# Kernel tuning notes

Hardware: AMD Instinct MI355X
Metric: run time of the kernel (lower is better)

## Reference

```python
import jax, jax.numpy as jnp
import numpy as np

NEG_SLOPE = 0.2
NUM_NODES = 100000
NUM_EDGES = 200000
NNZ = 1600000
IN_C = 128
OUT_C = 128
STAR = 64


def setup_inputs() -> dict:
    key = jax.random.key(0)
    ks = jax.random.split(key, 12)
    X = jax.random.normal(ks[0], (NUM_NODES, IN_C), dtype=jnp.float32)
    V = jax.random.randint(ks[1], (NNZ,), 0, NUM_NODES)
    E = jax.random.randint(ks[2], (NNZ,), 0, NUM_EDGES)
    S_features = jax.random.normal(ks[3], (NUM_EDGES, STAR), dtype=jnp.float32)
    s = 1.0 / np.sqrt(IN_C)
    Wx = jax.random.uniform(ks[4], (IN_C, OUT_C), minval=-s, maxval=s)
    bx = jax.random.uniform(ks[5], (OUT_C,), minval=-s, maxval=s)
    Wv = jax.random.uniform(ks[6], (IN_C, OUT_C), minval=-s, maxval=s)
    bv = jax.random.uniform(ks[7], (OUT_C,), minval=-s, maxval=s)
    sa = 1.0 / np.sqrt(OUT_C)
    a_vec = jax.random.uniform(ks[8], (OUT_C,), minval=-sa, maxval=sa)
    st = 1.0 / np.sqrt(OUT_C + STAR)
    Wt = jax.random.uniform(ks[9], (OUT_C + STAR, OUT_C), minval=-st, maxval=st)
    bt = jax.random.uniform(ks[10], (OUT_C,), minval=-st, maxval=st)
    return {"X": X, "V": V, "E": E, "S_features": S_features,
            "Wx": Wx, "bx": bx, "Wv": Wv, "bv": bv,
            "a_vec": a_vec, "Wt": Wt, "bt": bt}


def _segment_softmax(s, seg, num_segments):
    m = jax.ops.segment_max(s, seg, num_segments=num_segments)
    e = jnp.exp(s - m[seg])
    denom = jax.ops.segment_sum(e, seg, num_segments=num_segments)
    return e / denom[seg]


def reference(X, V, E, S_features, Wx, bx, Wv, bv, a_vec, Wt, bt):
    # DPHGNNConv forward (eval mode: dropout = identity)
    X_init = X @ Wx + bx                      # [N, out]
    X_feat = X @ Wv + bv                      # [N, out]
    scores = X_feat @ a_vec                   # [N]
    s = jax.nn.leaky_relu(scores[V], NEG_SLOPE)  # [nnz]
    w = _segment_softmax(s, E, NUM_EDGES)     # [nnz]
    Xev = X_feat[V] * w[:, None]              # [nnz, out]
    Y_v2e = jax.ops.segment_sum(Xev, E, num_segments=NUM_EDGES)
    Y_v2e = jax.nn.elu(Y_v2e)
    e_msg = jnp.concatenate([Y_v2e, S_features], axis=1)  # [E, out+star]
    Y = e_msg @ Wt + bt                       # [E, out]
    Yev = Y[E]                                # [nnz, out]
    num = jax.ops.segment_sum(Yev, V, num_segments=NUM_NODES)
    cnt = jax.ops.segment_sum(jnp.ones((NNZ,), jnp.float32), V, num_segments=NUM_NODES)
    Xn = num / jnp.maximum(cnt, 1.0)[:, None]  # scatter_mean
    Xn = jax.nn.elu(Xn)                        # is_last=False
    return Xn + X_init
```

## Files before the change

kernel.cpp:

```cpp
#include <hip/hip_runtime.h>
#include <math.h>

#define N_NODES 100000
#define N_EDGES 200000
#define NNZ_    1600000
#define INC  128
#define OUTC 128
#define STAR_ 64
#define NEG 0.2f
#define NBIN_E 391
#define NBIN_V 196
#define NBIN (NBIN_E + NBIN_V)
#define CHUNK 4000
#define CAP_E 5120
#define CAP_V 9216
#define PAIR_SZ (NBIN_E*CAP_E + NBIN_V*CAP_V)
#define CAPI 288

typedef __attribute__((ext_vector_type(8))) short bf16x8_t;
typedef __attribute__((ext_vector_type(4))) float f32x4_t;

__device__ __forceinline__ float leaky(float x){ return x > 0.f ? x : NEG*x; }
__device__ __forceinline__ float elu1(float x){ return x > 0.f ? x : __expf(x)-1.f; }
__device__ __forceinline__ unsigned short f2bf(float f){
  unsigned u = __float_as_uint(f);
  unsigned r = u + 0x7FFFu + ((u >> 16) & 1u);
  return (unsigned short)(r >> 16);
}
__device__ __forceinline__ float bf2f(unsigned short h){
  return __uint_as_float(((unsigned)h) << 16);
}
__device__ __forceinline__ int padBaseD(int bin){
  return bin < NBIN_E ? bin*CAP_E : NBIN_E*CAP_E + (bin-NBIN_E)*CAP_V;
}

__global__ void k_cvt(const float* __restrict__ Wx, const float* __restrict__ Wv,
                      const float* __restrict__ Wt,
                      unsigned short* __restrict__ WcatT, unsigned short* __restrict__ WtT,
                      int* __restrict__ binCur){
  const int i = blockIdx.x*256 + threadIdx.x;
  if (i < 256*128){
    const int n = i >> 7, k = i & 127;
    const float v = (n < 128) ? Wx[k*128 + n] : Wv[k*128 + (n-128)];
    WcatT[n*128 + k] = f2bf(v);
  }
  const int j = i - 256*128;
  if (j >= 0 && j < 128*192){
    const int n = j / 192, k = j - n*192;
    WtT[n*192 + k] = f2bf(Wt[k*128 + n]);
  }
  if (blockIdx.x == 0){
    for (int p = threadIdx.x; p < NBIN; p += 256) binCur[p] = padBaseD(p);
  }
}

__global__ __launch_bounds__(256) void k_gemm1(const float* __restrict__ X,
    const unsigned short* __restrict__ WcatT,
    const float* __restrict__ bx, const float* __restrict__ bv,
    float* __restrict__ Xinit, unsigned short* __restrict__ Xfb){
  __shared__ unsigned short xb[16][136];
  const int tid = threadIdx.x;
  const int lane = tid & 63, w = tid >> 6;
  const int quad = lane >> 4, l16 = lane & 15;
  const int r0 = blockIdx.x * 16;
  {
    const int r = tid >> 4;
    const int c0 = (tid & 15) * 8;
    const float4 a4 = *(const float4*)&X[(size_t)(r0+r)*INC + c0];
    const float4 b4 = *(const float4*)&X[(size_t)(r0+r)*INC + c0 + 4];
    bf16x8_t pk;
    pk[0]=(short)f2bf(a4.x); pk[1]=(short)f2bf(a4.y); pk[2]=(short)f2bf(a4.z); pk[3]=(short)f2bf(a4.w);
    pk[4]=(short)f2bf(b4.x); pk[5]=(short)f2bf(b4.y); pk[6]=(short)f2bf(b4.z); pk[7]=(short)f2bf(b4.w);
    *(bf16x8_t*)&xb[r][c0] = pk;
  }
  __syncthreads();
  f32x4_t acc[4] = {{0,0,0,0},{0,0,0,0},{0,0,0,0},{0,0,0,0}};
  const int n_base = w*64 + l16;
  for (int s = 0; s < 4; ++s){
    const bf16x8_t af = *(const bf16x8_t*)&xb[l16][s*32 + quad*8];
    #pragma unroll
    for (int nt = 0; nt < 4; ++nt){
      const int n = n_base + nt*16;
      const bf16x8_t bf = *(const bf16x8_t*)&WcatT[(size_t)n*128 + s*32 + quad*8];
      acc[nt] = __builtin_amdgcn_mfma_f32_16x16x32_bf16(af, bf, acc[nt], 0, 0, 0);
    }
  }
  #pragma unroll
  for (int nt = 0; nt < 4; ++nt){
    const int n = n_base + nt*16;
    const float bias = (n < 128) ? bx[n] : bv[n-128];
    #pragma unroll
    for (int r = 0; r < 4; ++r){
      const int m = quad*4 + r;
      const float val = acc[nt][r] + bias;
      if (n < 128) Xinit[(size_t)(r0+m)*OUTC + n] = val;
      else         Xfb[(size_t)(r0+m)*OUTC + (n-128)] = f2bf(val);
    }
  }
}

__global__ __launch_bounds__(256) void k_scores(const unsigned short* __restrict__ Xfb,
    const float* __restrict__ a, float* __restrict__ scores){
  const int lane = threadIdx.x & 63;
  const int w = threadIdx.x >> 6;
  const int r = blockIdx.x * 4 + w;
  const unsigned pair = *(const unsigned*)&Xfb[(size_t)r*OUTC + lane*2];
  float p = bf2f((unsigned short)(pair & 0xffff)) * a[lane*2]
          + bf2f((unsigned short)(pair >> 16))    * a[lane*2+1];
  #pragma unroll
  for (int o = 32; o; o >>= 1) p += __shfl_xor(p, o, 64);
  if (lane == 0) scores[r] = p;
}


__global__ __launch_bounds__(256) void k_binA(const int* __restrict__ V, const int* __restrict__ E,
                                              int* __restrict__ binCur, int2* __restrict__ pair){
  __shared__ int h[NBIN];
  __shared__ int base[NBIN];
  for (int p = threadIdx.x; p < NBIN; p += 256) h[p] = 0;
  __syncthreads();
  const int start = blockIdx.x*CHUNK, end = start + CHUNK;
  for (int i = start + threadIdx.x; i < end; i += 256){
    atomicAdd(&h[E[i] >> 9], 1);
    atomicAdd(&h[NBIN_E + (V[i] >> 9)], 1);
  }
  __syncthreads();
  for (int p = threadIdx.x; p < NBIN; p += 256)
    base[p] = h[p] ? atomicAdd(&binCur[p], h[p]) : 0;
  __syncthreads();
  for (int p = threadIdx.x; p < NBIN; p += 256) h[p] = 0;
  __syncthreads();
  for (int i = start + threadIdx.x; i < end; i += 256){
    const int e = E[i], v = V[i];
    const int be = e >> 9, bv = NBIN_E + (v >> 9);
    const int se = base[be] + atomicAdd(&h[be], 1);
    const int sv = base[bv] + atomicAdd(&h[bv], 1);
    pair[se] = make_int2(e, v);
    pair[sv] = make_int2(v, e);
  }
}

__global__ __launch_bounds__(1024) void k_binscan(const int* __restrict__ binCur,
                                                  int* __restrict__ binBase, int* __restrict__ binCnt,
                                                  int2* __restrict__ vw, int* __restrict__ eIdxV){
  __shared__ int s[1024];
  const int tid = threadIdx.x;
  const int v = (tid < NBIN) ? (binCur[tid] - padBaseD(tid)) : 0;
  s[tid] = v; __syncthreads();
  for (int o = 1; o < 1024; o <<= 1){
    const int u = (tid >= o) ? s[tid-o] : 0;
    __syncthreads();
    s[tid] += u;
    __syncthreads();
  }
  if (tid < NBIN){ binBase[tid] = s[tid] - v; binCnt[tid] = v; }
  if (tid < 16){ vw[NNZ_ + tid] = make_int2(0, 0); eIdxV[NNZ_ + tid] = 0; }
}

__global__ __launch_bounds__(256) void k_binB(const int2* __restrict__ pair,
    const int* __restrict__ binBase, const int* __restrict__ binCnt,
    const float* __restrict__ scores,
    int2* __restrict__ vw, int* __restrict__ eIdxV,
    int* __restrict__ cntE, int* __restrict__ startsE,
    int* __restrict__ cntV, int* __restrict__ startsV,
    float* __restrict__ dens){
  __shared__ int h[512], sc0[512], sc1[512];
  __shared__ float dsh[512];
  const int bin = blockIdx.x;
  const bool isE = bin < NBIN_E;
  const int nb = isE ? bin : bin - NBIN_E;
  const int bucket0 = nb << 9;
  const int nBuckTot = isE ? N_EDGES : N_NODES;
  const int pstart = padBaseD(bin);
  const int n = binCnt[bin];
  const int itemBase = isE ? binBase[bin] : binBase[bin] - NNZ_;
  const int tid = threadIdx.x;
  for (int p = tid; p < 512; p += 256){ h[p] = 0; dsh[p] = 0.f; }
  __syncthreads();
  for (int j = tid; j < n; j += 256) atomicAdd(&h[pair[pstart + j].x & 511], 1);
  __syncthreads();
  for (int p = tid; p < 512; p += 256) sc0[p] = h[p];
  __syncthreads();
  int* a = sc0; int* b = sc1;
  for (int o = 1; o < 512; o <<= 1){
    for (int p = tid; p < 512; p += 256) b[p] = a[p] + (p >= o ? a[p-o] : 0);
    __syncthreads();
    int* t = a; a = b; b = t;
  }
  for (int p = tid; p < 512; p += 256){
    const int excl = a[p] - h[p];
    b[p] = itemBase + excl;
    const int bucket = bucket0 + p;
    if (bucket < nBuckTot){
      if (isE){ cntE[bucket] = h[p]; startsE[bucket] = itemBase + excl; }
      else    { cntV[bucket] = h[p]; startsV[bucket] = itemBase + excl; }
    }
  }
  __syncthreads();
  for (int j = tid; j < n; j += 256){
    const int2 kv = pair[pstart + j];
    const int slot = atomicAdd(&b[kv.x & 511], 1);
    if (isE){
      const float ex = __expf(leaky(scores[kv.y]));
      vw[slot] = make_int2(kv.y, __float_as_int(ex));
      atomicAdd(&dsh[kv.x & 511], ex);
    } else {
      eIdxV[slot] = kv.y;
    }
  }
  __syncthreads();
  if (isE){
    for (int p = tid; p < 512; p += 256){
      const int bucket = bucket0 + p;
      if (bucket < N_EDGES) dens[bucket] = dsh[p];
    }
  }
}

__global__ __launch_bounds__(256) void k_edge(
    const int* __restrict__ cntE, const int* __restrict__ startsE,
    const int2* __restrict__ vw, const float* __restrict__ dens,
    const unsigned short* __restrict__ Xfb,
    const float* __restrict__ S, const unsigned short* __restrict__ WtT,
    const float* __restrict__ bt, unsigned short* __restrict__ Ybf) {
  __shared__ int2 inc[CAPI + 8];
  __shared__ unsigned short msg[16][200];
  const int tid = threadIdx.x;
  const int lane = tid & 63, w = tid >> 6;
  const int e0 = blockIdx.x * 16;
  const int sub = tid & 31, grp = tid >> 5;

  const int st0 = startsE[e0];
  const int lim = startsE[e0 + 15] + cntE[e0 + 15] - st0;

  for (int i = tid; i < CAPI + 8; i += 256)
    inc[i] = (i < lim) ? vw[st0 + i] : make_int2(0, 0);

  if (sub < 16) {
    const int cs = sub * 4;
    #pragma unroll
    for (int tt = 0; tt < 2; ++tt) {
      const int t = grp*2 + tt;
      const float4 s4 = *(const float4*)&S[(size_t)(e0+t)*STAR_ + cs];
      ushort4 pk; pk.x=f2bf(s4.x); pk.y=f2bf(s4.y); pk.z=f2bf(s4.z); pk.w=f2bf(s4.w);
      *(ushort4*)&msg[t][128 + cs] = pk;
    }
  }
  __syncthreads();

  const int c4 = sub * 4;
  #pragma unroll
  for (int tt = 0; tt < 2; ++tt) {
    const int t = grp*2 + tt;
    const int e = e0 + t;
    const int deg = cntE[e];
    const int lo  = startsE[e] - st0;
    float a0=0.f, a1=0.f, a2=0.f, a3=0.f;
    if (lo + deg <= CAPI) {
      for (int j = 0; j < deg; j += 8) {
        int2 pp[8];
        #pragma unroll
        for (int k = 0; k < 8; ++k) pp[k] = inc[lo + j + k];
        ushort4 xx[8];
        #pragma unroll
        for (int k = 0; k < 8; ++k)
          xx[k] = *(const ushort4*)&Xfb[(size_t)pp[k].x*OUTC + c4];
        #pragma unroll
        for (int k = 0; k < 8; ++k) {
          const float wgt = (j + k < deg) ? __int_as_float(pp[k].y) : 0.f;
          a0 += wgt * bf2f(xx[k].x); a1 += wgt * bf2f(xx[k].y);
          a2 += wgt * bf2f(xx[k].z); a3 += wgt * bf2f(xx[k].w);
        }
      }
    } else {
      const int st = st0 + lo;
      for (int j = 0; j < deg; j += 8) {
        int2 pp[8];
        #pragma unroll
        for (int k = 0; k < 8; ++k) pp[k] = vw[st + j + k];
        ushort4 xx[8];
        #pragma unroll
        for (int k = 0; k < 8; ++k)
          xx[k] = *(const ushort4*)&Xfb[(size_t)pp[k].x*OUTC + c4];
        #pragma unroll
        for (int k = 0; k < 8; ++k) {
          const float wgt = (j + k < deg) ? __int_as_float(pp[k].y) : 0.f;
          a0 += wgt * bf2f(xx[k].x); a1 += wgt * bf2f(xx[k].y);
          a2 += wgt * bf2f(xx[k].z); a3 += wgt * bf2f(xx[k].w);
        }
      }
    }
    const float invd = deg > 0 ? 1.f/dens[e] : 0.f;
    ushort4 pk;
    pk.x = f2bf(elu1(a0*invd)); pk.y = f2bf(elu1(a1*invd));
    pk.z = f2bf(elu1(a2*invd)); pk.w = f2bf(elu1(a3*invd));
    *(ushort4*)&msg[t][c4] = pk;
  }
  __syncthreads();

  const int quad = lane >> 4, l16 = lane & 15;
  f32x4_t acc0 = {0,0,0,0}, acc1 = {0,0,0,0};
  const int n0 = w * 32;
  for (int s = 0; s < 6; ++s) {
    const bf16x8_t af = *(const bf16x8_t*)&msg[l16][s*32 + quad*8];
    const bf16x8_t b0 = *(const bf16x8_t*)&WtT[(size_t)(n0 + l16)*192      + s*32 + quad*8];
    const bf16x8_t b1 = *(const bf16x8_t*)&WtT[(size_t)(n0 + 16 + l16)*192 + s*32 + quad*8];
    acc0 = __builtin_amdgcn_mfma_f32_16x16x32_bf16(af, b0, acc0, 0, 0, 0);
    acc1 = __builtin_amdgcn_mfma_f32_16x16x32_bf16(af, b1, acc1, 0, 0, 0);
  }
  const float bt0 = bt[n0 + l16], bt1 = bt[n0 + 16 + l16];
  #pragma unroll
  for (int r = 0; r < 4; ++r) {
    const int m = quad*4 + r;
    Ybf[(size_t)(e0+m)*OUTC + n0 + l16]      = f2bf(acc0[r] + bt0);
    Ybf[(size_t)(e0+m)*OUTC + n0 + 16 + l16] = f2bf(acc1[r] + bt1);
  }
}

__global__ __launch_bounds__(256) void k_node(
    const int* __restrict__ cntV, const int* __restrict__ startsV,
    const int* __restrict__ eIdxV,
    const unsigned short* __restrict__ Ybf, float* __restrict__ out) {
  __shared__ int elds[CAPI + 8];
  const int tid = threadIdx.x;
  const int sub = tid & 31, grp = tid >> 5;
  const int v0 = blockIdx.x * 8;

  const int st0 = startsV[v0];
  const int lim = startsV[v0 + 7] + cntV[v0 + 7] - st0;
  for (int i = tid; i < CAPI + 8; i += 256)
    elds[i] = (i < lim) ? eIdxV[st0 + i] : 0;
  __syncthreads();

  const int v = v0 + grp;
  const int c4 = sub * 4;
  const int deg = cntV[v];
  const int lo  = startsV[v] - st0;
  float a0=0.f, a1=0.f, a2=0.f, a3=0.f;
  if (lo + deg <= CAPI) {
    for (int j = 0; j < deg; j += 8) {
      int ee[8];
      #pragma unroll
      for (int k = 0; k < 8; ++k) ee[k] = elds[lo + j + k];
      ushort4 yy[8];
      #pragma unroll
      for (int k = 0; k < 8; ++k)
        yy[k] = *(const ushort4*)&Ybf[(size_t)ee[k]*OUTC + c4];
      #pragma unroll
      for (int k = 0; k < 8; ++k) {
        const float pz = (j + k < deg) ? 1.f : 0.f;
        a0 += pz * bf2f(yy[k].x); a1 += pz * bf2f(yy[k].y);
        a2 += pz * bf2f(yy[k].z); a3 += pz * bf2f(yy[k].w);
      }
    }
  } else {
    const int st = st0 + lo;
    for (int j = 0; j < deg; j += 8) {
      int ee[8];
      #pragma unroll
      for (int k = 0; k < 8; ++k) ee[k] = eIdxV[st + j + k];
      ushort4 yy[8];
      #pragma unroll
      for (int k = 0; k < 8; ++k)
        yy[k] = *(const ushort4*)&Ybf[(size_t)ee[k]*OUTC + c4];
      #pragma unroll
      for (int k = 0; k < 8; ++k) {
        const float pz = (j + k < deg) ? 1.f : 0.f;
        a0 += pz * bf2f(yy[k].x); a1 += pz * bf2f(yy[k].y);
        a2 += pz * bf2f(yy[k].z); a3 += pz * bf2f(yy[k].w);
      }
    }
  }
  const float invd = 1.f / fmaxf((float)deg, 1.f);
  float4 o = *(float4*)&out[(size_t)v*OUTC + c4];
  o.x = elu1(a0*invd) + o.x;
  o.y = elu1(a1*invd) + o.y;
  o.z = elu1(a2*invd) + o.z;
  o.w = elu1(a3*invd) + o.w;
  *(float4*)&out[(size_t)v*OUTC + c4] = o;
}

extern "C" void kernel_launch(void* const* d_in, const int* in_sizes, int n_in,
                              void* d_out, int out_size, void* d_ws, size_t ws_size,
                              hipStream_t stream) {
  const float* X  = (const float*)d_in[0];
  const int*   V  = (const int*)d_in[1];
  const int*   E  = (const int*)d_in[2];
  const float* S  = (const float*)d_in[3];
  const float* Wx = (const float*)d_in[4];
  const float* bx = (const float*)d_in[5];
  const float* Wv = (const float*)d_in[6];
  const float* bv = (const float*)d_in[7];
  const float* av = (const float*)d_in[8];
  const float* Wt = (const float*)d_in[9];
  const float* bt = (const float*)d_in[10];
  float* out = (float*)d_out;

  char* ws = (char*)d_ws;
  size_t off = 0;
  auto alloc = [&](size_t bytes) -> void* {
    off = (off + 255) & ~(size_t)255;
    void* p = ws + off; off += bytes; return p;
  };
  unsigned short* Xfb   = (unsigned short*)alloc((size_t)N_NODES*OUTC*2);
  unsigned short* Ybf   = (unsigned short*)alloc((size_t)N_EDGES*OUTC*2);
  float* scores = (float*)alloc((size_t)N_NODES*4);
  unsigned short* WcatT = (unsigned short*)alloc((size_t)256*128*2);
  unsigned short* WtT   = (unsigned short*)alloc((size_t)128*192*2);
  int2* pair   = (int2*)alloc((size_t)PAIR_SZ*8);
  int* binBase = (int*)alloc((size_t)NBIN*4);
  int* binCur  = (int*)alloc((size_t)NBIN*4);
  int* binCnt  = (int*)alloc((size_t)NBIN*4);
  int* cntE    = (int*)alloc((size_t)N_EDGES*4);
  int* cntV    = (int*)alloc((size_t)N_NODES*4);
  int* startsE = (int*)alloc((size_t)N_EDGES*4);
  int* startsV = (int*)alloc((size_t)N_NODES*4);
  int2* vw     = (int2*)alloc((size_t)(NNZ_+16)*8);
  int* eIdxV   = (int*)alloc((size_t)(NNZ_+16)*4);
  float* dens  = (float*)alloc((size_t)N_EDGES*4);

  k_cvt<<<(256*128 + 128*192 + 255)/256, 256, 0, stream>>>(Wx, Wv, Wt, WcatT, WtT, binCur);
  k_gemm1<<<N_NODES/16, 256, 0, stream>>>(X, WcatT, bx, bv, out, Xfb);
  k_scores<<<N_NODES/4, 256, 0, stream>>>(Xfb, av, scores);

  k_binA<<<NNZ_/CHUNK, 256, 0, stream>>>(V, E, binCur, pair);
  k_binscan<<<1, 1024, 0, stream>>>(binCur, binBase, binCnt, vw, eIdxV);
  k_binB<<<NBIN, 256, 0, stream>>>(pair, binBase, binCnt, scores, vw, eIdxV,
                                   cntE, startsE, cntV, startsV, dens);

  k_edge<<<N_EDGES/16, 256, 0, stream>>>(cntE, startsE, vw, dens, Xfb, S, WtT, bt, Ybf);
  k_node<<<N_NODES/8, 256, 0, stream>>>(cntV, startsV, eIdxV, Ybf, out);
}
```

Measured before the change: 497.9 us.

## Fuse score dot-product into GEMM epilogue and widen gathers to 16B per lane

Removes the separate k_scores launch by computing the attention score dot product inside the k_gemm1 epilogue, using shared-memory atomics across waves. The edge and node gather kernels now use 16 lanes per row with 8-element (16-byte) bf16 loads instead of 32 lanes with 4-element loads. The node kernel also processes 16 nodes per block with a larger LDS index cache. Scores are now computed from fp32 values before bf16 rounding, which slightly changes numerics. The wider per-lane accumulators raise register pressure, and there are fewer lanes in flight per row.

```diff
diff --git a/kernel.cpp b/kernel.cpp
--- a/kernel.cpp
+++ b/kernel.cpp
@@ -16,8 +16,10 @@
 #define CAP_V 9216
 #define PAIR_SZ (NBIN_E*CAP_E + NBIN_V*CAP_V)
 #define CAPI 288
+#define CAPN 448
 
 typedef __attribute__((ext_vector_type(8))) short bf16x8_t;
+typedef __attribute__((ext_vector_type(8))) unsigned short u16x8;
 typedef __attribute__((ext_vector_type(4))) float f32x4_t;
 
 __device__ __forceinline__ float leaky(float x){ return x > 0.f ? x : NEG*x; }
@@ -57,12 +59,16 @@
 __global__ __launch_bounds__(256) void k_gemm1(const float* __restrict__ X,
     const unsigned short* __restrict__ WcatT,
     const float* __restrict__ bx, const float* __restrict__ bv,
-    float* __restrict__ Xinit, unsigned short* __restrict__ Xfb){
+    const float* __restrict__ av,
+    float* __restrict__ Xinit, unsigned short* __restrict__ Xfb,
+    float* __restrict__ scores){
   __shared__ unsigned short xb[16][136];
+  __shared__ float sc[16];
   const int tid = threadIdx.x;
   const int lane = tid & 63, w = tid >> 6;
   const int quad = lane >> 4, l16 = lane & 15;
   const int r0 = blockIdx.x * 16;
+  if (tid < 16) sc[tid] = 0.f;
   {
     const int r = tid >> 4;
     const int c0 = (tid & 15) * 8;
@@ -85,6 +91,7 @@
       acc[nt] = __builtin_amdgcn_mfma_f32_16x16x32_bf16(af, bf, acc[nt], 0, 0, 0);
     }
   }
+  float pr[4] = {0.f, 0.f, 0.f, 0.f};
   #pragma unroll
   for (int nt = 0; nt < 4; ++nt){
     const int n = n_base + nt*16;
@@ -94,22 +101,18 @@
       const int m = quad*4 + r;
       const float val = acc[nt][r] + bias;
       if (n < 128) Xinit[(size_t)(r0+m)*OUTC + n] = val;
-      else         Xfb[(size_t)(r0+m)*OUTC + (n-128)] = f2bf(val);
-    }
-  }
-}
-
-__global__ __launch_bounds__(256) void k_scores(const unsigned short* __restrict__ Xfb,
-    const float* __restrict__ a, float* __restrict__ scores){
-  const int lane = threadIdx.x & 63;
-  const int w = threadIdx.x >> 6;
-  const int r = blockIdx.x * 4 + w;
-  const unsigned pair = *(const unsigned*)&Xfb[(size_t)r*OUTC + lane*2];
-  float p = bf2f((unsigned short)(pair & 0xffff)) * a[lane*2]
-          + bf2f((unsigned short)(pair >> 16))    * a[lane*2+1];
-  #pragma unroll
-  for (int o = 32; o; o >>= 1) p += __shfl_xor(p, o, 64);
-  if (lane == 0) scores[r] = p;
+      else {
+        Xfb[(size_t)(r0+m)*OUTC + (n-128)] = f2bf(val);
+        pr[r] += val * av[n-128];
+      }
+    }
+  }
+  if (w >= 2){
+    #pragma unroll
+    for (int r = 0; r < 4; ++r) atomicAdd(&sc[quad*4 + r], pr[r]);
+  }
+  __syncthreads();
+  if (tid < 16) scores[r0 + tid] = sc[tid];
 }
 
 
@@ -228,7 +231,7 @@
   const int tid = threadIdx.x;
   const int lane = tid & 63, w = tid >> 6;
   const int e0 = blockIdx.x * 16;
-  const int sub = tid & 31, grp = tid >> 5;
+  const int g16 = tid >> 4, s16 = tid & 15;
 
   const int st0 = startsE[e0];
   const int lim = startsE[e0 + 15] + cntE[e0 + 15] - st0;
@@ -236,65 +239,58 @@
   for (int i = tid; i < CAPI + 8; i += 256)
     inc[i] = (i < lim) ? vw[st0 + i] : make_int2(0, 0);
 
-  if (sub < 16) {
-    const int cs = sub * 4;
+  {
+    const float4 s4 = *(const float4*)&S[(size_t)(e0+g16)*STAR_ + s16*4];
+    ushort4 pk; pk.x=f2bf(s4.x); pk.y=f2bf(s4.y); pk.z=f2bf(s4.z); pk.w=f2bf(s4.w);
+    *(ushort4*)&msg[g16][128 + s16*4] = pk;
+  }
+  __syncthreads();
+
+  const int e = e0 + g16;
+  const int deg = cntE[e];
+  const int lo  = startsE[e] - st0;
+  const int c8 = s16 * 8;
+  float ac[8] = {0.f,0.f,0.f,0.f,0.f,0.f,0.f,0.f};
+  if (lo + deg <= CAPI) {
+    for (int j = 0; j < deg; j += 8) {
+      int2 pp[8];
+      #pragma unroll
+      for (int k = 0; k < 8; ++k) pp[k] = inc[lo + j + k];
+      u16x8 xx[8];
+      #pragma unroll
+      for (int k = 0; k < 8; ++k)
+        xx[k] = *(const u16x8*)&Xfb[(size_t)pp[k].x*OUTC + c8];
+      #pragma unroll
+      for (int k = 0; k < 8; ++k) {
+        const float wgt = (j + k < deg) ? __int_as_float(pp[k].y) : 0.f;
+        #pragma unroll
+        for (int q = 0; q < 8; ++q) ac[q] += wgt * bf2f(xx[k][q]);
+      }
+    }
+  } else {
+    const int st = st0 + lo;
+    for (int j = 0; j < deg; j += 8) {
+      int2 pp[8];
+      #pragma unroll
+      for (int k = 0; k < 8; ++k) pp[k] = vw[st + j + k];
+      u16x8 xx[8];
+      #pragma unroll
+      for (int k = 0; k < 8; ++k)
+        xx[k] = *(const u16x8*)&Xfb[(size_t)pp[k].x*OUTC + c8];
+      #pragma unroll
+      for (int k = 0; k < 8; ++k) {
+        const float wgt = (j + k < deg) ? __int_as_float(pp[k].y) : 0.f;
+        #pragma unroll
+        for (int q = 0; q < 8; ++q) ac[q] += wgt * bf2f(xx[k][q]);
+      }
+    }
+  }
+  {
+    const float invd = deg > 0 ? 1.f/dens[e] : 0.f;
+    u16x8 pk;
     #pragma unroll
-    for (int tt = 0; tt < 2; ++tt) {
-      const int t = grp*2 + tt;
-      const float4 s4 = *(const float4*)&S[(size_t)(e0+t)*STAR_ + cs];
-      ushort4 pk; pk.x=f2bf(s4.x); pk.y=f2bf(s4.y); pk.z=f2bf(s4.z); pk.w=f2bf(s4.w);
-      *(ushort4*)&msg[t][128 + cs] = pk;
-    }
-  }
-  __syncthreads();
-
-  const int c4 = sub * 4;
-  #pragma unroll
-  for (int tt = 0; tt < 2; ++tt) {
-    const int t = grp*2 + tt;
-    const int e = e0 + t;
-    const int deg = cntE[e];
-    const int lo  = startsE[e] - st0;
-    float a0=0.f, a1=0.f, a2=0.f, a3=0.f;
-    if (lo + deg <= CAPI) {
-      for (int j = 0; j < deg; j += 8) {
-        int2 pp[8];
-        #pragma unroll
-        for (int k = 0; k < 8; ++k) pp[k] = inc[lo + j + k];
-        ushort4 xx[8];
-        #pragma unroll
-        for (int k = 0; k < 8; ++k)
-          xx[k] = *(const ushort4*)&Xfb[(size_t)pp[k].x*OUTC + c4];
-        #pragma unroll
-        for (int k = 0; k < 8; ++k) {
-          const float wgt = (j + k < deg) ? __int_as_float(pp[k].y) : 0.f;
-          a0 += wgt * bf2f(xx[k].x); a1 += wgt * bf2f(xx[k].y);
-          a2 += wgt * bf2f(xx[k].z); a3 += wgt * bf2f(xx[k].w);
-        }
-      }
-    } else {
-      const int st = st0 + lo;
-      for (int j = 0; j < deg; j += 8) {
-        int2 pp[8];
-        #pragma unroll
-        for (int k = 0; k < 8; ++k) pp[k] = vw[st + j + k];
-        ushort4 xx[8];
-        #pragma unroll
-        for (int k = 0; k < 8; ++k)
-          xx[k] = *(const ushort4*)&Xfb[(size_t)pp[k].x*OUTC + c4];
-        #pragma unroll
-        for (int k = 0; k < 8; ++k) {
-          const float wgt = (j + k < deg) ? __int_as_float(pp[k].y) : 0.f;
-          a0 += wgt * bf2f(xx[k].x); a1 += wgt * bf2f(xx[k].y);
-          a2 += wgt * bf2f(xx[k].z); a3 += wgt * bf2f(xx[k].w);
-        }
-      }
-    }
-    const float invd = deg > 0 ? 1.f/dens[e] : 0.f;
-    ushort4 pk;
-    pk.x = f2bf(elu1(a0*invd)); pk.y = f2bf(elu1(a1*invd));
-    pk.z = f2bf(elu1(a2*invd)); pk.w = f2bf(elu1(a3*invd));
-    *(ushort4*)&msg[t][c4] = pk;
+    for (int q = 0; q < 8; ++q) pk[q] = f2bf(elu1(ac[q]*invd));
+    *(u16x8*)&msg[g16][c8] = pk;
   }
   __syncthreads();
 
@@ -321,36 +317,36 @@
     const int* __restrict__ cntV, const int* __restrict__ startsV,
     const int* __restrict__ eIdxV,
     const unsigned short* __restrict__ Ybf, float* __restrict__ out) {
-  __shared__ int elds[CAPI + 8];
+  __shared__ int elds[CAPN + 8];
   const int tid = threadIdx.x;
-  const int sub = tid & 31, grp = tid >> 5;
-  const int v0 = blockIdx.x * 8;
+  const int g16 = tid >> 4, s16 = tid & 15;
+  const int v0 = blockIdx.x * 16;
 
   const int st0 = startsV[v0];
-  const int lim = startsV[v0 + 7] + cntV[v0 + 7] - st0;
-  for (int i = tid; i < CAPI + 8; i += 256)
+  const int lim = startsV[v0 + 15] + cntV[v0 + 15] - st0;
+  for (int i = tid; i < CAPN + 8; i += 256)
     elds[i] = (i < lim) ? eIdxV[st0 + i] : 0;
   __syncthreads();
 
-  const int v = v0 + grp;
-  const int c4 = sub * 4;
+  const int v = v0 + g16;
   const int deg = cntV[v];
   const int lo  = startsV[v] - st0;
-  float a0=0.f, a1=0.f, a2=0.f, a3=0.f;
-  if (lo + deg <= CAPI) {
+  const int c8 = s16 * 8;
+  float ac[8] = {0.f,0.f,0.f,0.f,0.f,0.f,0.f,0.f};
+  if (lo + deg <= CAPN) {
     for (int j = 0; j < deg; j += 8) {
       int ee[8];
       #pragma unroll
       for (int k = 0; k < 8; ++k) ee[k] = elds[lo + j + k];
-      ushort4 yy[8];
+      u16x8 yy[8];
       #pragma unroll
       for (int k = 0; k < 8; ++k)
-        yy[k] = *(const ushort4*)&Ybf[(size_t)ee[k]*OUTC + c4];
+        yy[k] = *(const u16x8*)&Ybf[(size_t)ee[k]*OUTC + c8];
       #pragma unroll
       for (int k = 0; k < 8; ++k) {
         const float pz = (j + k < deg) ? 1.f : 0.f;
-        a0 += pz * bf2f(yy[k].x); a1 += pz * bf2f(yy[k].y);
-        a2 += pz * bf2f(yy[k].z); a3 += pz * bf2f(yy[k].w);
+        #pragma unroll
+        for (int q = 0; q < 8; ++q) ac[q] += pz * bf2f(yy[k][q]);
       }
     }
   } else {
@@ -359,25 +355,31 @@
       int ee[8];
       #pragma unroll
       for (int k = 0; k < 8; ++k) ee[k] = eIdxV[st + j + k];
-      ushort4 yy[8];
+      u16x8 yy[8];
       #pragma unroll
       for (int k = 0; k < 8; ++k)
-        yy[k] = *(const ushort4*)&Ybf[(size_t)ee[k]*OUTC + c4];
+        yy[k] = *(const u16x8*)&Ybf[(size_t)ee[k]*OUTC + c8];
       #pragma unroll
       for (int k = 0; k < 8; ++k) {
         const float pz = (j + k < deg) ? 1.f : 0.f;
-        a0 += pz * bf2f(yy[k].x); a1 += pz * bf2f(yy[k].y);
-        a2 += pz * bf2f(yy[k].z); a3 += pz * bf2f(yy[k].w);
+        #pragma unroll
+        for (int q = 0; q < 8; ++q) ac[q] += pz * bf2f(yy[k][q]);
       }
     }
   }
   const float invd = 1.f / fmaxf((float)deg, 1.f);
-  float4 o = *(float4*)&out[(size_t)v*OUTC + c4];
-  o.x = elu1(a0*invd) + o.x;
-  o.y = elu1(a1*invd) + o.y;
-  o.z = elu1(a2*invd) + o.z;
-  o.w = elu1(a3*invd) + o.w;
-  *(float4*)&out[(size_t)v*OUTC + c4] = o;
+  float4 o0 = *(float4*)&out[(size_t)v*OUTC + c8];
+  float4 o1 = *(float4*)&out[(size_t)v*OUTC + c8 + 4];
+  o0.x = elu1(ac[0]*invd) + o0.x;
+  o0.y = elu1(ac[1]*invd) + o0.y;
+  o0.z = elu1(ac[2]*invd) + o0.z;
+  o0.w = elu1(ac[3]*invd) + o0.w;
+  o1.x = elu1(ac[4]*invd) + o1.x;
+  o1.y = elu1(ac[5]*invd) + o1.y;
+  o1.z = elu1(ac[6]*invd) + o1.z;
+  o1.w = elu1(ac[7]*invd) + o1.w;
+  *(float4*)&out[(size_t)v*OUTC + c8]     = o0;
+  *(float4*)&out[(size_t)v*OUTC + c8 + 4] = o1;
 }
 
 extern "C" void kernel_launch(void* const* d_in, const int* in_sizes, int n_in,
@@ -420,8 +422,7 @@
   float* dens  = (float*)alloc((size_t)N_EDGES*4);
 
   k_cvt<<<(256*128 + 128*192 + 255)/256, 256, 0, stream>>>(Wx, Wv, Wt, WcatT, WtT, binCur);
-  k_gemm1<<<N_NODES/16, 256, 0, stream>>>(X, WcatT, bx, bv, out, Xfb);
-  k_scores<<<N_NODES/4, 256, 0, stream>>>(Xfb, av, scores);
+  k_gemm1<<<N_NODES/16, 256, 0, stream>>>(X, WcatT, bx, bv, av, out, Xfb, scores);
 
   k_binA<<<NNZ_/CHUNK, 256, 0, stream>>>(V, E, binCur, pair);
   k_binscan<<<1, 1024, 0, stream>>>(binCur, binBase, binCnt, vw, eIdxV);
@@ -429,5 +430,5 @@
                                    cntE, startsE, cntV, startsV, dens);
 
   k_edge<<<N_EDGES/16, 256, 0, stream>>>(cntE, startsE, vw, dens, Xfb, S, WtT, bt, Ybf);
-  k_node<<<N_NODES/8, 256, 0, stream>>>(cntV, startsV, eIdxV, Ybf, out);
-}
+  k_node<<<N_NODES/16, 256, 0, stream>>>(cntV, startsV, eIdxV, Ybf, out);
+}
```

After: 513.4 us. +3.1%, slower.
